# Kernel tuning notes

Hardware: AMD Instinct MI355X
Metric: run time of the kernel (lower is better)

## Reference

```python
import jax, jax.numpy as jnp
import numpy as np

SIGMA_MAX = 25.0

def marginal_prob_std(t):
    # VE-SDE std: sqrt((sigma_max^(2t) - 1) / (2 ln sigma_max))
    log_s = jnp.log(SIGMA_MAX)
    return jnp.sqrt((jnp.exp(2.0 * t * log_s) - 1.0) / (2.0 * log_s))

def setup_inputs() -> dict:
    key = jax.random.key(0)
    k1, k2, k3 = jax.random.split(key, 3)
    B, N, d = 16384, 16384, 1
    x = jax.random.normal(k1, (B, d), dtype=jnp.float32)
    t = jax.random.uniform(k2, (B,), dtype=jnp.float32, minval=1e-3, maxval=1.0)
    train_data = jax.random.normal(k3, (N, d), dtype=jnp.float32)
    return {"x": x, "t": t, "train_data": train_data}

def reference(x, t, train_data):
    # x: [B,1], t: [B], train_data: [N,1]
    sigma = marginal_prob_std(t)                       # [B]
    sigma2 = sigma * sigma                             # [B]
    # pairwise squared distance (d=1): [N, B]
    diff = train_data - x[:, 0][None, :]               # [N,1]-[1,B] -> broadcast fails; do explicit
    diff = train_data[:, 0][:, None] - x[:, 0][None, :]  # [N, B]
    pdf = jnp.exp(-0.5 * (diff * diff) / sigma2[None, :])  # [N, B]
    num = jnp.sum(pdf * train_data, axis=0)            # [N,B]*[N,1] -> [B]
    den = jnp.sum(pdf, axis=0)                         # [B]
    den_safe = jnp.where(den == 0.0, 1.0, den)
    evals = jnp.where(den == 0.0, 0.0, num / den_safe) # nan -> 0 as in torch code
    evals = evals[:, None]                             # [B,1]
    return (evals - x) / sigma2[:, None]
```

## Files before the change

### kernel.cpp

```cpp
#include <hip/hip_runtime.h>
#include <math.h>


typedef float v2f __attribute__((ext_vector_type(2)));

#define BLK   256
#define JB    16
#define PARTS 16

#if __has_builtin(__builtin_amdgcn_exp2f)
#define EXP2(x) __builtin_amdgcn_exp2f(x)
#else
#define EXP2(x) exp2f(x)
#endif

__device__ __forceinline__ float sigma2_of(float tj) {
  const float TWO_LOG_S = 6.4377516497364011f;
  return (__expf(TWO_LOG_S * tj) - 1.0f) / TWO_LOG_S;
}

__launch_bounds__(BLK, 4)
__global__ void gmm_fused(const float* __restrict__ x,
                          const float* __restrict__ t,
                          const float* __restrict__ td,
                          float* __restrict__ out,
                          int N, int B) {
  __shared__ float nbuf[PARTS * JB];
  __shared__ float dbuf[PARTS * JB];

  const int tid  = threadIdx.x;
  const int jl   = tid & (JB - 1);
  const int part = tid >> 4;
  const int j    = blockIdx.x * JB + jl;

  const int W  = (N + PARTS - 1) / PARTS;
  const int lo = part * W;
  const int hi = (lo + W < N) ? (lo + W) : N;

  float r = 0.0f, y = 0.0f;
  if (j < B) {
    const float HALF_LOG2E = 0.72134752044448170f;
    float s2 = sigma2_of(t[j]);
    r = __fsqrt_rn(HALF_LOG2E / s2);
    y = x[j] * r;
  }

  const v2f rv  = {r, r};
  const v2f nyv = {-y, -y};

  v2f n0 = {0.f, 0.f}, n1 = {0.f, 0.f};
  v2f d0 = {0.f, 0.f}, d1 = {0.f, 0.f};

#define GROUP(v, nacc, dacc)                                            \
  {                                                                     \
    v2f dd = __builtin_elementwise_fma(v, rv, nyv);                     \
    v2f qq = dd * dd;                                                   \
    v2f pp;                                                             \
    pp.x = EXP2(-qq.x); pp.y = EXP2(-qq.y);                             \
    dacc += pp;                                                         \
    nacc = __builtin_elementwise_fma(pp, v, nacc);                      \
  }

  int i = lo;
  if (((W & 3) == 0)) {
    const int hi8 = lo + ((hi - lo) & ~7);
    #pragma unroll 2
    for (; i < hi8; i += 8) {
      float4 v0 = *(const float4*)(td + i);
      float4 v1 = *(const float4*)(td + i + 4);
      v2f va = {v0.x, v0.y}, vb = {v0.z, v0.w};
      v2f vc = {v1.x, v1.y}, vd = {v1.z, v1.w};
      GROUP(va, n0, d0)
      GROUP(vb, n1, d1)
      GROUP(vc, n0, d0)
      GROUP(vd, n1, d1)
    }
  }
  for (; i < hi; i += 2) {
    float e0 = td[i];
    float e1 = (i + 1 < hi) ? td[i + 1] : 1e30f;
    v2f v = {e0, e1};
    GROUP(v, n0, d0)
  }
#undef GROUP

  v2f numv = n0 + n1;
  v2f denv = d0 + d1;
  nbuf[part * JB + jl] = numv.x + numv.y;
  dbuf[part * JB + jl] = denv.x + denv.y;
  __syncthreads();

  if (tid < JB && (blockIdx.x * JB + tid) < B) {
    const int jj = blockIdx.x * JB + tid;
    float num = 0.f, den = 0.f;
    #pragma unroll
    for (int p = 0; p < PARTS; ++p) {
      num += nbuf[p * JB + tid];
      den += dbuf[p * JB + tid];
    }
    float sigma2 = sigma2_of(t[jj]);
    float evals = (den == 0.0f) ? 0.0f : (num / den);
    out[jj] = (evals - x[jj]) / sigma2;
  }
}

extern "C" void kernel_launch(void* const* d_in, const int* in_sizes, int n_in,
                              void* d_out, int out_size, void* d_ws, size_t ws_size,
                              hipStream_t stream) {
  const float* x  = (const float*)d_in[0];
  const float* t  = (const float*)d_in[1];
  const float* td = (const float*)d_in[2];
  float* out = (float*)d_out;
  (void)d_ws; (void)ws_size;

  const int B = in_sizes[0];
  const int N = in_sizes[2];

  const int GX = (B + JB - 1) / JB;
  gmm_fused<<<GX, BLK, 0, stream>>>(x, t, td, out, N, B);
}
```

Before: 95.13 us.

## Stage train_data chunks through LDS with register prefetch instead of direct global loads

Each block now loads 2048-element chunks of train_data cooperatively into shared memory, prefetching the next chunk into registers while computing on the current one. Each part reads interleaved float4s from LDS rather than its own contiguous global slice, and four accumulator pairs replace two to lengthen independent dependency chains. This aims to replace per-thread redundant global/L1 loads with LDS reads, at the cost of two barriers per chunk and an extra LDS write pass. Because the kernel is dominated by exp2 work and the data was already L1/L2 resident, the benefit is uncertain.

```diff
diff --git a/kernel.cpp b/kernel.cpp
--- a/kernel.cpp
+++ b/kernel.cpp
@@ -7,6 +7,7 @@
 #define BLK   256
 #define JB    16
 #define PARTS 16
+#define CH    2048
 
 #if __has_builtin(__builtin_amdgcn_exp2f)
 #define EXP2(x) __builtin_amdgcn_exp2f(x)
@@ -19,12 +20,24 @@
   return (__expf(TWO_LOG_S * tj) - 1.0f) / TWO_LOG_S;
 }
 
+__device__ __forceinline__ float4 load_pad(const float* __restrict__ td,
+                                           int gi, int N) {
+  if (gi + 3 < N) return *(const float4*)(td + gi);
+  float4 v;
+  v.x = (gi + 0 < N) ? td[gi + 0] : 1e30f;
+  v.y = (gi + 1 < N) ? td[gi + 1] : 1e30f;
+  v.z = (gi + 2 < N) ? td[gi + 2] : 1e30f;
+  v.w = (gi + 3 < N) ? td[gi + 3] : 1e30f;
+  return v;
+}
+
 __launch_bounds__(BLK, 4)
 __global__ void gmm_fused(const float* __restrict__ x,
                           const float* __restrict__ t,
                           const float* __restrict__ td,
                           float* __restrict__ out,
                           int N, int B) {
+  __shared__ float lds[CH];
   __shared__ float nbuf[PARTS * JB];
   __shared__ float dbuf[PARTS * JB];
 
@@ -32,10 +45,6 @@
   const int jl   = tid & (JB - 1);
   const int part = tid >> 4;
   const int j    = blockIdx.x * JB + jl;
-
-  const int W  = (N + PARTS - 1) / PARTS;
-  const int lo = part * W;
-  const int hi = (lo + W < N) ? (lo + W) : N;
 
   float r = 0.0f, y = 0.0f;
   if (j < B) {
@@ -48,8 +57,8 @@
   const v2f rv  = {r, r};
   const v2f nyv = {-y, -y};
 
-  v2f n0 = {0.f, 0.f}, n1 = {0.f, 0.f};
-  v2f d0 = {0.f, 0.f}, d1 = {0.f, 0.f};
+  v2f n0 = {0.f, 0.f}, n1 = {0.f, 0.f}, n2 = {0.f, 0.f}, n3 = {0.f, 0.f};
+  v2f d0 = {0.f, 0.f}, d1 = {0.f, 0.f}, d2 = {0.f, 0.f}, d3 = {0.f, 0.f};
 
 #define GROUP(v, nacc, dacc)                                            \
   {                                                                     \
@@ -61,31 +70,44 @@
     nacc = __builtin_elementwise_fma(pp, v, nacc);                      \
   }
 
-  int i = lo;
-  if (((W & 3) == 0)) {
-    const int hi8 = lo + ((hi - lo) & ~7);
-    #pragma unroll 2
-    for (; i < hi8; i += 8) {
-      float4 v0 = *(const float4*)(td + i);
-      float4 v1 = *(const float4*)(td + i + 4);
+  const int NC = (N + CH - 1) / CH;
+  const float4* l4 = (const float4*)lds;
+
+  float4 pA = load_pad(td, tid * 4, N);
+  float4 pB = load_pad(td, (tid + BLK) * 4, N);
+
+  for (int c = 0; c < NC; ++c) {
+    float4 nA = pA, nB = pB;
+    if (c + 1 < NC) {
+      const int nb = (c + 1) * CH;
+      nA = load_pad(td, nb + tid * 4, N);
+      nB = load_pad(td, nb + (tid + BLK) * 4, N);
+    }
+
+    ((float4*)lds)[tid]       = pA;
+    ((float4*)lds)[tid + BLK] = pB;
+    __syncthreads();
+
+    #pragma unroll 4
+    for (int k = 0; k < CH / 64; k += 2) {
+      float4 v0 = l4[part + 16 * k];
+      float4 v1 = l4[part + 16 * k + 16];
       v2f va = {v0.x, v0.y}, vb = {v0.z, v0.w};
       v2f vc = {v1.x, v1.y}, vd = {v1.z, v1.w};
       GROUP(va, n0, d0)
       GROUP(vb, n1, d1)
-      GROUP(vc, n0, d0)
-      GROUP(vd, n1, d1)
+      GROUP(vc, n2, d2)
+      GROUP(vd, n3, d3)
     }
-  }
-  for (; i < hi; i += 2) {
-    float e0 = td[i];
-    float e1 = (i + 1 < hi) ? td[i + 1] : 1e30f;
-    v2f v = {e0, e1};
-    GROUP(v, n0, d0)
+    __syncthreads();
+
+    pA = nA;
+    pB = nB;
   }
 #undef GROUP
 
-  v2f numv = n0 + n1;
-  v2f denv = d0 + d1;
+  v2f numv = (n0 + n1) + (n2 + n3);
+  v2f denv = (d0 + d1) + (d2 + d3);
   nbuf[part * JB + jl] = numv.x + numv.y;
   dbuf[part * JB + jl] = denv.x + denv.y;
   __syncthreads();
```

Measured after the change: 92.38 us. 2.9% less time.
